# Optimization experiments

Hardware: AMD Instinct MI355X
Metric: run time of the kernel (lower is better)

The kernel has to match this reference:

```python
import jax, jax.numpy as jnp
import numpy as np

L, D, FF, H, S, B = 6, 512, 2048, 8, 1024, 4
DH = D // H
EPS = 1e-5


def setup_inputs() -> dict:
    key = jax.random.key(0)
    ks = jax.random.split(key, 8)
    sd = 1.0 / np.sqrt(D)
    sf = 1.0 / np.sqrt(FF)
    return {
        'src': jax.random.normal(ks[0], (S, B, D), jnp.float32),
        'pos': jax.random.normal(ks[1], (S, B, D), jnp.float32) * 0.02,
        'Wq': jax.random.normal(ks[2], (L, D, D), jnp.float32) * sd,
        'bq': jnp.zeros((L, D), jnp.float32),
        'Wk': jax.random.normal(ks[3], (L, D, D), jnp.float32) * sd,
        'bk': jnp.zeros((L, D), jnp.float32),
        'Wv': jax.random.normal(ks[4], (L, D, D), jnp.float32) * sd,
        'bv': jnp.zeros((L, D), jnp.float32),
        'W1': jax.random.normal(ks[5], (L, D, FF), jnp.float32) * sd,
        'b1': jnp.zeros((L, FF), jnp.float32),
        'W2': jax.random.normal(ks[6], (L, FF, D), jnp.float32) * sf,
        'b2': jnp.zeros((L, D), jnp.float32),
        'ln1_g': jnp.ones((L, D), jnp.float32),
        'ln1_b': jnp.zeros((L, D), jnp.float32),
        'ln2_g': jnp.ones((L, D), jnp.float32),
        'ln2_b': jnp.zeros((L, D), jnp.float32),
        'lnf_g': jnp.ones((D,), jnp.float32),
        'lnf_b': jnp.zeros((D,), jnp.float32),
    }


def _layernorm(x, g, b):
    m = jnp.mean(x, axis=-1, keepdims=True)
    v = jnp.mean(jnp.square(x - m), axis=-1, keepdims=True)
    return (x - m) * jax.lax.rsqrt(v + EPS) * g + b


def _encoder(src, pos, Wq, bq, Wk, bk, Wv, bv, W1, b1, W2, b2,
             ln1_g, ln1_b, ln2_g, ln2_b, lnf_g, lnf_b):
    # src, pos: (S, B, D). Each layer internally transposes to (B, S, D) and the
    # encoder transposes back; equivalently work in (B, S, D) throughout the loop.
    x = (src + pos).transpose(1, 0, 2)  # (B, S, D)
    scale = 1.0 / np.sqrt(DH)
    for i in range(L):
        # --- self-attention block (pre-norm) ---
        x1 = _layernorm(x, ln1_g[i], ln1_b[i])
        q = (x1 @ Wq[i] + bq[i]).reshape(B, S, H, DH)
        k = (x1 @ Wk[i] + bk[i]).reshape(B, S, H, DH)
        v = (x1 @ Wv[i] + bv[i]).reshape(B, S, H, DH)
        scores = jnp.einsum('bqhd,bkhd->bhqk', q, k) * scale  # (B, H, S, S)
        probs = jax.nn.softmax(scores, axis=-1)
        ctx = jnp.einsum('bhqk,bkhd->bqhd', probs, v).reshape(B, S, D)
        x = x + ctx  # dropout=0.0 -> identity
        # --- feed-forward block (pre-norm) ---
        x2 = _layernorm(x, ln2_g[i], ln2_b[i])
        h = jax.nn.relu(x2 @ W1[i] + b1[i])
        x = x + (h @ W2[i] + b2[i])
    out = x.transpose(1, 0, 2)  # back to (S, B, D)
    return _layernorm(out, lnf_g, lnf_b)


def reference(src, pos, Wq, bq, Wk, bk, Wv, bv, W1, b1, W2, b2,
              ln1_g, ln1_b, ln2_g, ln2_b, lnf_g, lnf_b):
    return _encoder(src, pos, Wq, bq, Wk, bk, Wv, bv, W1, b1, W2, b2,
                    ln1_g, ln1_b, ln2_g, ln2_b, lnf_g, lnf_b)
```

## Files before the change

kernel.cpp:

```cpp
#include <hip/hip_runtime.h>

#define L_LAYERS 6
#define DMODEL 512
#define FFDIM 2048
#define NHEAD 8
#define SEQ 1024
#define BATCH 4
#define DHEAD 64
#define MROWS (BATCH*SEQ)

typedef __attribute__((ext_vector_type(4))) float f32x4;
typedef __attribute__((ext_vector_type(8))) unsigned short u16x8;
typedef __attribute__((ext_vector_type(8))) __bf16 bf16x8;

#define DEV static __device__ __forceinline__

DEV unsigned short f32_to_bf16(float f) {
  unsigned int u = __float_as_uint(f);
  u += 0x7fffu + ((u >> 16) & 1u);
  return (unsigned short)(u >> 16);
}
DEV float bf16_to_f32(unsigned short h) {
  return __uint_as_float(((unsigned int)h) << 16);
}
DEV f32x4 mfma_bf16(u16x8 a, u16x8 b, f32x4 c) {
  return __builtin_amdgcn_mfma_f32_16x16x32_bf16(
      __builtin_bit_cast(bf16x8, a), __builtin_bit_cast(bf16x8, b), c, 0, 0, 0);
}
DEV void gload16(const unsigned short* g, unsigned short* l) {
  __builtin_amdgcn_global_load_lds(
      (const __attribute__((address_space(1))) unsigned int*)g,
      (__attribute__((address_space(3))) unsigned int*)l, 16, 0, 0);
}

__global__ __launch_bounds__(256) void k_transpose(const float* __restrict__ Win,
                                                   unsigned short* __restrict__ Wout,
                                                   int K, int N) {
  __shared__ float t[32][33];
  Win  += (size_t)blockIdx.z * K * N;
  Wout += (size_t)blockIdx.z * K * N;
  int n0 = blockIdx.x * 32, k0 = blockIdx.y * 32;
  int lx = threadIdx.x & 31, ly = threadIdx.x >> 5;
  #pragma unroll
  for (int r = 0; r < 32; r += 8)
    t[ly + r][lx] = Win[(size_t)(k0 + ly + r) * N + n0 + lx];
  __syncthreads();
  #pragma unroll
  for (int r = 0; r < 32; r += 8)
    Wout[(size_t)(n0 + ly + r) * K + k0 + lx] = f32_to_bf16(t[lx][ly + r]);
}

__global__ __launch_bounds__(256) void k_addpos_ln(const float* __restrict__ src,
                                                   const float* __restrict__ pos,
                                                   const float* __restrict__ g,
                                                   const float* __restrict__ be,
                                                   float* __restrict__ x,
                                                   unsigned short* __restrict__ o) {
  int lane = threadIdx.x & 63, wv = threadIdx.x >> 6;
  int row = blockIdx.x * 4 + wv;
  int b = row >> 10, ss = row & (SEQ-1);
  const float* sr = src + (size_t)(ss*BATCH + b) * DMODEL + lane * 8;
  const float* pr = pos + (size_t)(ss*BATCH + b) * DMODEL + lane * 8;
  f32x4 v0 = *(const f32x4*)sr + *(const f32x4*)pr;
  f32x4 v1 = *(const f32x4*)(sr + 4) + *(const f32x4*)(pr + 4);
  float* xr = x + (size_t)row * DMODEL + lane * 8;
  *(f32x4*)xr = v0;
  *(f32x4*)(xr + 4) = v1;
  float s  = v0.x+v0.y+v0.z+v0.w + v1.x+v1.y+v1.z+v1.w;
  float s2 = v0.x*v0.x+v0.y*v0.y+v0.z*v0.z+v0.w*v0.w
           + v1.x*v1.x+v1.y*v1.y+v1.z*v1.z+v1.w*v1.w;
  #pragma unroll
  for (int off = 1; off < 64; off <<= 1) { s += __shfl_xor(s, off); s2 += __shfl_xor(s2, off); }
  float mean = s * (1.0f/DMODEL);
  float var  = s2 * (1.0f/DMODEL) - mean*mean;
  float rs = rsqrtf(var + 1e-5f);
  const float* gp = g + lane*8; const float* bp = be + lane*8;
  f32x4 g0 = *(const f32x4*)gp, g1 = *(const f32x4*)(gp+4);
  f32x4 b0 = *(const f32x4*)bp, b1v = *(const f32x4*)(bp+4);
  u16x8 r;
  r[0] = f32_to_bf16((v0.x-mean)*rs*g0.x + b0.x);
  r[1] = f32_to_bf16((v0.y-mean)*rs*g0.y + b0.y);
  r[2] = f32_to_bf16((v0.z-mean)*rs*g0.z + b0.z);
  r[3] = f32_to_bf16((v0.w-mean)*rs*g0.w + b0.w);
  r[4] = f32_to_bf16((v1.x-mean)*rs*g1.x + b1v.x);
  r[5] = f32_to_bf16((v1.y-mean)*rs*g1.y + b1v.y);
  r[6] = f32_to_bf16((v1.z-mean)*rs*g1.z + b1v.z);
  r[7] = f32_to_bf16((v1.w-mean)*rs*g1.w + b1v.w);
  *(u16x8*)(o + (size_t)row * DMODEL + lane * 8) = r;
}

__global__ __launch_bounds__(256) void k_ln_bf16(const float* __restrict__ x,
                                                 const float* __restrict__ g,
                                                 const float* __restrict__ be,
                                                 unsigned short* __restrict__ o) {
  int lane = threadIdx.x & 63, wv = threadIdx.x >> 6;
  int row = blockIdx.x * 4 + wv;
  const float* xr = x + (size_t)row * DMODEL + lane * 8;
  f32x4 v0 = *(const f32x4*)xr, v1 = *(const f32x4*)(xr + 4);
  float s  = v0.x+v0.y+v0.z+v0.w + v1.x+v1.y+v1.z+v1.w;
  float s2 = v0.x*v0.x+v0.y*v0.y+v0.z*v0.z+v0.w*v0.w
           + v1.x*v1.x+v1.y*v1.y+v1.z*v1.z+v1.w*v1.w;
  #pragma unroll
  for (int off = 1; off < 64; off <<= 1) { s += __shfl_xor(s, off); s2 += __shfl_xor(s2, off); }
  float mean = s * (1.0f/DMODEL);
  float var  = s2 * (1.0f/DMODEL) - mean*mean;
  float rs = rsqrtf(var + 1e-5f);
  const float* gp = g + lane*8; const float* bp = be + lane*8;
  f32x4 g0 = *(const f32x4*)gp, g1 = *(const f32x4*)(gp+4);
  f32x4 b0 = *(const f32x4*)bp, b1v = *(const f32x4*)(bp+4);
  u16x8 r;
  r[0] = f32_to_bf16((v0.x-mean)*rs*g0.x + b0.x);
  r[1] = f32_to_bf16((v0.y-mean)*rs*g0.y + b0.y);
  r[2] = f32_to_bf16((v0.z-mean)*rs*g0.z + b0.z);
  r[3] = f32_to_bf16((v0.w-mean)*rs*g0.w + b0.w);
  r[4] = f32_to_bf16((v1.x-mean)*rs*g1.x + b1v.x);
  r[5] = f32_to_bf16((v1.y-mean)*rs*g1.y + b1v.y);
  r[6] = f32_to_bf16((v1.z-mean)*rs*g1.z + b1v.z);
  r[7] = f32_to_bf16((v1.w-mean)*rs*g1.w + b1v.w);
  *(u16x8*)(o + (size_t)row * DMODEL + lane * 8) = r;
}

__global__ __launch_bounds__(256) void k_ln_final(const float* __restrict__ x,
                                                  const float* __restrict__ g,
                                                  const float* __restrict__ be,
                                                  float* __restrict__ out) {
  int lane = threadIdx.x & 63, wv = threadIdx.x >> 6;
  int row = blockIdx.x * 4 + wv;
  const float* xr = x + (size_t)row * DMODEL + lane * 8;
  f32x4 v0 = *(const f32x4*)xr, v1 = *(const f32x4*)(xr + 4);
  float s  = v0.x+v0.y+v0.z+v0.w + v1.x+v1.y+v1.z+v1.w;
  float s2 = v0.x*v0.x+v0.y*v0.y+v0.z*v0.z+v0.w*v0.w
           + v1.x*v1.x+v1.y*v1.y+v1.z*v1.z+v1.w*v1.w;
  #pragma unroll
  for (int off = 1; off < 64; off <<= 1) { s += __shfl_xor(s, off); s2 += __shfl_xor(s2, off); }
  float mean = s * (1.0f/DMODEL);
  float var  = s2 * (1.0f/DMODEL) - mean*mean;
  float rs = rsqrtf(var + 1e-5f);
  const float* gp = g + lane*8; const float* bp = be + lane*8;
  f32x4 g0 = *(const f32x4*)gp, g1 = *(const f32x4*)(gp+4);
  f32x4 b0 = *(const f32x4*)bp, b1v = *(const f32x4*)(bp+4);
  int b = row >> 10, ss = row & (SEQ-1);
  float* orow = out + (size_t)(ss*BATCH + b) * DMODEL + lane * 8;
  f32x4 o0, o1;
  o0.x = (v0.x-mean)*rs*g0.x + b0.x;  o0.y = (v0.y-mean)*rs*g0.y + b0.y;
  o0.z = (v0.z-mean)*rs*g0.z + b0.z;  o0.w = (v0.w-mean)*rs*g0.w + b0.w;
  o1.x = (v1.x-mean)*rs*g1.x + b1v.x; o1.y = (v1.y-mean)*rs*g1.y + b1v.y;
  o1.z = (v1.z-mean)*rs*g1.z + b1v.z; o1.w = (v1.w-mean)*rs*g1.w + b1v.w;
  *(f32x4*)orow = o0;
  *(f32x4*)(orow + 4) = o1;
}

#define BM 128
#define BN 128
#define BKK 32

DEV void gemm_core(const unsigned short* __restrict__ A,
                   const unsigned short* __restrict__ Bt,
                   int K, int m0, int n0,
                   unsigned short* As, unsigned short* Bs, f32x4 acc[4][4]) {
  const int tid = threadIdx.x;
  const int lane = tid & 63;
  const int w = tid >> 6;
  const int wr = w >> 1, wc = w & 1;
  const int l15 = lane & 15;
  const int ko = (lane >> 4) * 8;
  const int rl = lane >> 2;
  const int cc = (lane & 3) * 8;
  for (int kb = 0; kb < K; kb += BKK) {
    #pragma unroll
    for (int i = 0; i < 2; ++i) {
      int r0 = w * 32 + i * 16;
      gload16(A  + (size_t)(m0 + r0 + rl) * K + kb + cc, As + r0 * BKK);
      gload16(Bt + (size_t)(n0 + r0 + rl) * K + kb + cc, Bs + r0 * BKK);
    }
    __syncthreads();
    u16x8 af[4], bfr[4];
    #pragma unroll
    for (int m = 0; m < 4; ++m) af[m]  = *(const u16x8*)(As + (wr*64 + m*16 + l15) * BKK + ko);
    #pragma unroll
    for (int n = 0; n < 4; ++n) bfr[n] = *(const u16x8*)(Bs + (wc*64 + n*16 + l15) * BKK + ko);
    #pragma unroll
    for (int m = 0; m < 4; ++m)
      #pragma unroll
      for (int n = 0; n < 4; ++n)
        acc[m][n] = mfma_bf16(af[m], bfr[n], acc[m][n]);
    __syncthreads();
  }
}

__global__ __launch_bounds__(256) void k_gemm_qkv(
    const unsigned short* __restrict__ x1,
    const unsigned short* __restrict__ WqT, const unsigned short* __restrict__ WkT,
    const unsigned short* __restrict__ WvT,
    const float* __restrict__ bq, const float* __restrict__ bk, const float* __restrict__ bv,
    unsigned short* __restrict__ qo, unsigned short* __restrict__ ko2,
    unsigned short* __restrict__ vo) {
  __shared__ __align__(16) unsigned short As[BM*BKK];
  __shared__ __align__(16) unsigned short Bs[64*BKK];
  const int tid = threadIdx.x;
  const int lane = tid & 63;
  const int w = tid >> 6;
  const int wr = w >> 1, wc = w & 1;
  const int l15 = lane & 15;
  const int ko = (lane >> 4) * 8;
  const int rl = lane >> 2;
  const int cc = (lane & 3) * 8;
  const int m0 = blockIdx.x * BM;
  const int mat = blockIdx.y >> 3;
  const int n0 = (blockIdx.y & 7) * 64;
  const unsigned short* Bt = (mat == 0) ? WqT : ((mat == 1) ? WkT : WvT);
  const float* bias        = (mat == 0) ? bq  : ((mat == 1) ? bk  : bv);
  unsigned short* out      = (mat == 0) ? qo  : ((mat == 1) ? ko2 : vo);
  const float osc = (mat == 0) ? 0.125f : 1.0f;
  f32x4 acc[4][2];
  #pragma unroll
  for (int m = 0; m < 4; ++m)
    #pragma unroll
    for (int n = 0; n < 2; ++n) acc[m][n] = 0.0f;
  for (int kb = 0; kb < DMODEL; kb += BKK) {
    #pragma unroll
    for (int i = 0; i < 2; ++i) {
      int r0 = w * 32 + i * 16;
      gload16(x1 + (size_t)(m0 + r0 + rl) * DMODEL + kb + cc, As + r0 * BKK);
    }
    {
      int r0 = w * 16;
      gload16(Bt + (size_t)(n0 + r0 + rl) * DMODEL + kb + cc, Bs + r0 * BKK);
    }
    __syncthreads();
    u16x8 af[4], bfr[2];
    #pragma unroll
    for (int m = 0; m < 4; ++m) af[m]  = *(const u16x8*)(As + (wr*64 + m*16 + l15) * BKK + ko);
    #pragma unroll
    for (int n = 0; n < 2; ++n) bfr[n] = *(const u16x8*)(Bs + (wc*32 + n*16 + l15) * BKK + ko);
    #pragma unroll
    for (int m = 0; m < 4; ++m)
      #pragma unroll
      for (int n = 0; n < 2; ++n)
        acc[m][n] = mfma_bf16(af[m], bfr[n], acc[m][n]);
    __syncthreads();
  }
  const int g = lane >> 4;
  #pragma unroll
  for (int m = 0; m < 4; ++m) {
    #pragma unroll
    for (int n = 0; n < 2; ++n) {
      int col = n0 + wc*32 + n*16 + l15;
      int hh = col >> 6, dh = col & 63;
      float bval = bias[col];
      #pragma unroll
      for (int i = 0; i < 4; ++i) {
        int row = m0 + wr*64 + m*16 + g*4 + i;
        int bb = row >> 10, ss = row & (SEQ-1);
        size_t oidx;
        if (mat == 2)
          oidx = ((((size_t)(bb*NHEAD + hh)) * DHEAD + dh) << 10) + ss;
        else
          oidx = ((((size_t)(bb*NHEAD + hh)) << 10) + ss) * DHEAD + dh;
        out[oidx] = f32_to_bf16((acc[m][n][i] + bval) * osc);
      }
    }
  }
}

__global__ __launch_bounds__(256) void k_gemm_ffn1(
    const unsigned short* __restrict__ x1, const unsigned short* __restrict__ W1T,
    const float* __restrict__ b1, unsigned short* __restrict__ h) {
  __shared__ __align__(16) unsigned short As[BM*BKK];
  __shared__ __align__(16) unsigned short Bs[BN*BKK];
  int m0 = blockIdx.x * BM, n0 = blockIdx.y * BN;
  f32x4 acc[4][4];
  #pragma unroll
  for (int m = 0; m < 4; ++m)
    #pragma unroll
    for (int n = 0; n < 4; ++n) acc[m][n] = 0.0f;
  gemm_core(x1, W1T, DMODEL, m0, n0, As, Bs, acc);
  const int lane = threadIdx.x & 63;
  const int w = threadIdx.x >> 6; const int wr = w >> 1, wc = w & 1;
  #pragma unroll
  for (int m = 0; m < 4; ++m) {
    #pragma unroll
    for (int n = 0; n < 4; ++n) {
      int col = n0 + wc*64 + n*16 + (lane & 15);
      float bval = b1[col];
      #pragma unroll
      for (int i = 0; i < 4; ++i) {
        int row = m0 + wr*64 + m*16 + (lane >> 4)*4 + i;
        h[(size_t)row * FFDIM + col] = f32_to_bf16(fmaxf(acc[m][n][i] + bval, 0.0f));
      }
    }
  }
}

__global__ __launch_bounds__(256) void k_gemm_ffn2(
    const unsigned short* __restrict__ h, const unsigned short* __restrict__ W2T,
    const float* __restrict__ b2, float* __restrict__ x) {
  __shared__ __align__(16) unsigned short As[64*BKK];
  __shared__ __align__(16) unsigned short Bs[64*BKK];
  const int tid = threadIdx.x;
  const int lane = tid & 63;
  const int w = tid >> 6;
  const int wr = w >> 1, wc = w & 1;
  const int l15 = lane & 15;
  const int ko = (lane >> 4) * 8;
  const int rl = lane >> 2;
  const int cc = (lane & 3) * 8;
  const int m0 = blockIdx.x * 64, n0 = blockIdx.y * 64;
  f32x4 acc[2][2];
  #pragma unroll
  for (int m = 0; m < 2; ++m)
    #pragma unroll
    for (int n = 0; n < 2; ++n) acc[m][n] = 0.0f;
  for (int kb = 0; kb < FFDIM; kb += BKK) {
    int r0 = w * 16;
    gload16(h   + (size_t)(m0 + r0 + rl) * FFDIM + kb + cc, As + r0 * BKK);
    gload16(W2T + (size_t)(n0 + r0 + rl) * FFDIM + kb + cc, Bs + r0 * BKK);
    __syncthreads();
    u16x8 af[2], bfr[2];
    #pragma unroll
    for (int m = 0; m < 2; ++m) af[m]  = *(const u16x8*)(As + (wr*32 + m*16 + l15) * BKK + ko);
    #pragma unroll
    for (int n = 0; n < 2; ++n) bfr[n] = *(const u16x8*)(Bs + (wc*32 + n*16 + l15) * BKK + ko);
    #pragma unroll
    for (int m = 0; m < 2; ++m)
      #pragma unroll
      for (int n = 0; n < 2; ++n)
        acc[m][n] = mfma_bf16(af[m], bfr[n], acc[m][n]);
    __syncthreads();
  }
  const int g = lane >> 4;
  #pragma unroll
  for (int m = 0; m < 2; ++m) {
    #pragma unroll
    for (int n = 0; n < 2; ++n) {
      int col = n0 + wc*32 + n*16 + l15;
      float bval = b2[col];
      #pragma unroll
      for (int i = 0; i < 4; ++i) {
        int row = m0 + wr*32 + m*16 + g*4 + i;
        size_t idx = (size_t)row * DMODEL + col;
        x[idx] = x[idx] + acc[m][n][i] + bval;
      }
    }
  }
}

#define KVBLK 64
#define KP 72
#define NT (SEQ/KVBLK)
#define RESCALE_THR 8.0f

__global__ __launch_bounds__(512) void k_attn_mfma(
    const unsigned short* __restrict__ qb,
    const unsigned short* __restrict__ kb,
    const unsigned short* __restrict__ vtb,
    float* __restrict__ x) {
  __shared__ __align__(16) unsigned short Kl[2][KVBLK*KP];
  __shared__ __align__(16) unsigned short Vl[2][DHEAD*KP];
  __shared__ __align__(16) unsigned short Pl[8*16*KP];
  const int tid = threadIdx.x;
  const int w = tid >> 6, lane = tid & 63;
  const int c = lane & 15, g = lane >> 4;
  const int bh = blockIdx.x, qt = blockIdx.y;
  const int qw = qt * 128 + w * 16;
  const int sr = tid >> 3;
  const int scb = (tid & 7) * 8;

  const unsigned short* kbase = kb + (size_t)bh * SEQ * DHEAD;
  const unsigned short* vbase = vtb + (size_t)bh * DHEAD * SEQ;

  u16x8 qf[2];
  {
    const unsigned short* qrow = qb + ((size_t)bh * SEQ + qw + c) * DHEAD;
    qf[0] = *(const u16x8*)(qrow + g * 8);
    qf[1] = *(const u16x8*)(qrow + 32 + g * 8);
  }
  f32x4 aco[4];
  #pragma unroll
  for (int n = 0; n < 4; ++n) aco[n] = 0.0f;
  float m_r = -1e30f, l_r = 0.0f;

  u16x8 kr0, vr0;
  kr0 = *(const u16x8*)(kbase + (size_t)sr * DHEAD + scb);
  vr0 = *(const u16x8*)(vbase + (size_t)sr * SEQ + scb);
  *(u16x8*)(Kl[0] + sr * KP + scb) = kr0;
  *(u16x8*)(Vl[0] + sr * KP + scb) = vr0;
  __syncthreads();

  int cur = 0;
  for (int t = 0; t < NT; ++t) {
    if (t < NT - 1) {
      int kn = (t + 1) * KVBLK;
      kr0 = *(const u16x8*)(kbase + (size_t)(kn + sr) * DHEAD + scb);
      vr0 = *(const u16x8*)(vbase + (size_t)sr * SEQ + kn + scb);
    }
    const unsigned short* Kt = Kl[cur];
    const unsigned short* Vt = Vl[cur];

    f32x4 s[4];
    #pragma unroll
    for (int n = 0; n < 4; ++n) s[n] = 0.0f;
    #pragma unroll
    for (int n = 0; n < 4; ++n) {
      #pragma unroll
      for (int kk = 0; kk < 2; ++kk) {
        u16x8 kf = *(const u16x8*)(Kt + (n * 16 + c) * KP + kk * 32 + g * 8);
        s[n] = mfma_bf16(kf, qf[kk], s[n]);
      }
    }

    float mx01 = fmaxf(fmaxf(s[0][0], s[0][1]), fmaxf(s[0][2], s[0][3]));
    float mx1  = fmaxf(fmaxf(s[1][0], s[1][1]), fmaxf(s[1][2], s[1][3]));
    float mx2  = fmaxf(fmaxf(s[2][0], s[2][1]), fmaxf(s[2][2], s[2][3]));
    float mx3  = fmaxf(fmaxf(s[3][0], s[3][1]), fmaxf(s[3][2], s[3][3]));
    float mx = fmaxf(fmaxf(mx01, mx1), fmaxf(mx2, mx3));
    mx = fmaxf(mx, __shfl_xor(mx, 16));
    mx = fmaxf(mx, __shfl_xor(mx, 32));

    bool grow = !__all(mx <= m_r + RESCALE_THR);
    float corr = 1.0f;
    if (grow) {
      float mn = fmaxf(m_r, mx);
      corr = __expf(m_r - mn);
      m_r = mn;
    }

    float p[4][4];
    float ps = 0.0f;
    #pragma unroll
    for (int n = 0; n < 4; ++n) {
      #pragma unroll
      for (int i = 0; i < 4; ++i) {
        float pv = __expf(s[n][i] - m_r);
        p[n][i] = pv;
        ps += pv;
      }
    }
    ps += __shfl_xor(ps, 16);
    ps += __shfl_xor(ps, 32);
    l_r = l_r * corr + ps;

    {
      unsigned short* prow = Pl + (w * 16 + c) * KP;
      #pragma unroll
      for (int n = 0; n < 4; ++n) {
        unsigned int pk0 = (unsigned int)f32_to_bf16(p[n][0])
                         | ((unsigned int)f32_to_bf16(p[n][1]) << 16);
        unsigned int pk1 = (unsigned int)f32_to_bf16(p[n][2])
                         | ((unsigned int)f32_to_bf16(p[n][3]) << 16);
        *(unsigned int*)(prow + n * 16 + g * 4)     = pk0;
        *(unsigned int*)(prow + n * 16 + g * 4 + 2) = pk1;
      }
    }

    if (grow) {
      #pragma unroll
      for (int i = 0; i < 4; ++i) {
        float cq = __shfl(corr, g * 4 + i);
        #pragma unroll
        for (int n = 0; n < 4; ++n) aco[n][i] *= cq;
      }
    }

    u16x8 pa[2];
    pa[0] = *(const u16x8*)(Pl + (w * 16 + c) * KP + g * 8);
    pa[1] = *(const u16x8*)(Pl + (w * 16 + c) * KP + 32 + g * 8);
    #pragma unroll
    for (int n = 0; n < 4; ++n) {
      #pragma unroll
      for (int kk = 0; kk < 2; ++kk) {
        u16x8 vf = *(const u16x8*)(Vt + (n * 16 + c) * KP + kk * 32 + g * 8);
        aco[n] = mfma_bf16(pa[kk], vf, aco[n]);
      }
    }

    if (t < NT - 1) {
      unsigned short* Kn = Kl[cur ^ 1];
      unsigned short* Vn = Vl[cur ^ 1];
      *(u16x8*)(Kn + sr * KP + scb) = kr0;
      *(u16x8*)(Vn + sr * KP + scb) = vr0;
      __syncthreads();
    }
    cur ^= 1;
  }

  const int b = bh >> 3, h = bh & 7;
  #pragma unroll
  for (int i = 0; i < 4; ++i) {
    float lq = __shfl(l_r, g * 4 + i);
    float inv = 1.0f / lq;
    int q = qw + g * 4 + i;
    float* xr = x + ((size_t)b * SEQ + q) * DMODEL + h * DHEAD;
    #pragma unroll
    for (int n = 0; n < 4; ++n)
      xr[n * 16 + c] += aco[n][i] * inv;
  }
}

extern "C" void kernel_launch(void* const* d_in, const int* in_sizes, int n_in,
                              void* d_out, int out_size, void* d_ws, size_t ws_size,
                              hipStream_t stream) {
  const float* src  = (const float*)d_in[0];
  const float* pos  = (const float*)d_in[1];
  const float* Wq   = (const float*)d_in[2];
  const float* bq   = (const float*)d_in[3];
  const float* Wk   = (const float*)d_in[4];
  const float* bk   = (const float*)d_in[5];
  const float* Wv   = (const float*)d_in[6];
  const float* bv   = (const float*)d_in[7];
  const float* W1   = (const float*)d_in[8];
  const float* b1   = (const float*)d_in[9];
  const float* W2   = (const float*)d_in[10];
  const float* b2   = (const float*)d_in[11];
  const float* ln1g = (const float*)d_in[12];
  const float* ln1b = (const float*)d_in[13];
  const float* ln2g = (const float*)d_in[14];
  const float* ln2b = (const float*)d_in[15];
  const float* lnfg = (const float*)d_in[16];
  const float* lnfb = (const float*)d_in[17];

  char* p = (char*)d_ws;
  float* x = (float*)p;                      p += (size_t)MROWS * DMODEL * 4;
  unsigned short* x1 = (unsigned short*)p;   p += (size_t)MROWS * DMODEL * 2;
  unsigned short* qb = (unsigned short*)p;   p += (size_t)MROWS * DMODEL * 2;
  unsigned short* kbuf = (unsigned short*)p; p += (size_t)MROWS * DMODEL * 2;
  unsigned short* vtbuf = (unsigned short*)p; p += (size_t)MROWS * DMODEL * 2;
  unsigned short* hbuf = (unsigned short*)p; p += (size_t)MROWS * FFDIM * 2;
  unsigned short* WqT = (unsigned short*)p;  p += (size_t)L_LAYERS * DMODEL * DMODEL * 2;
  unsigned short* WkT = (unsigned short*)p;  p += (size_t)L_LAYERS * DMODEL * DMODEL * 2;
  unsigned short* WvT = (unsigned short*)p;  p += (size_t)L_LAYERS * DMODEL * DMODEL * 2;
  unsigned short* W1T = (unsigned short*)p;  p += (size_t)L_LAYERS * DMODEL * FFDIM * 2;
  unsigned short* W2T = (unsigned short*)p;  p += (size_t)L_LAYERS * DMODEL * FFDIM * 2;

  k_transpose<<<dim3(16,16,6), 256, 0, stream>>>(Wq, WqT, DMODEL, DMODEL);
  k_transpose<<<dim3(16,16,6), 256, 0, stream>>>(Wk, WkT, DMODEL, DMODEL);
  k_transpose<<<dim3(16,16,6), 256, 0, stream>>>(Wv, WvT, DMODEL, DMODEL);
  k_transpose<<<dim3(64,16,6), 256, 0, stream>>>(W1, W1T, DMODEL, FFDIM);
  k_transpose<<<dim3(16,64,6), 256, 0, stream>>>(W2, W2T, FFDIM, DMODEL);

  for (int l = 0; l < L_LAYERS; ++l) {
    if (l == 0)
      k_addpos_ln<<<1024, 256, 0, stream>>>(src, pos, ln1g, ln1b, x, x1);
    else
      k_ln_bf16<<<1024, 256, 0, stream>>>(x, ln1g + l*DMODEL, ln1b + l*DMODEL, x1);
    k_gemm_qkv<<<dim3(32,24), 256, 0, stream>>>(
        x1,
        WqT + (size_t)l*DMODEL*DMODEL, WkT + (size_t)l*DMODEL*DMODEL, WvT + (size_t)l*DMODEL*DMODEL,
        bq + l*DMODEL, bk + l*DMODEL, bv + l*DMODEL,
        qb, kbuf, vtbuf);
    k_attn_mfma<<<dim3(32,8), 512, 0, stream>>>(qb, kbuf, vtbuf, x);
    k_ln_bf16<<<1024, 256, 0, stream>>>(x, ln2g + l*DMODEL, ln2b + l*DMODEL, x1);
    k_gemm_ffn1<<<dim3(32,16), 256, 0, stream>>>(x1, W1T + (size_t)l*DMODEL*FFDIM, b1 + l*FFDIM, hbuf);
    k_gemm_ffn2<<<dim3(64,8), 256, 0, stream>>>(hbuf, W2T + (size_t)l*DMODEL*FFDIM, b2 + l*DMODEL, x);
  }
  k_ln_final<<<1024, 256, 0, stream>>>(x, lnfg, lnfb, (float*)d_out);
}
```

Before: 559.9 us.

## Switch attention kernel to 32x32x16 MFMA with 32-query waves

Rewrites the flash-attention kernel to use 32x32x16 bf16 MFMA instructions, with each of 4 waves handling 32 query rows instead of 8 waves handling 16. Row max and sum reductions need fewer cross-lane shuffles, and K/V fragments in LDS are reused across more queries per wave. The block shrinks to 256 threads and each thread stages two 16-byte chunks per tile. In exchange each wave holds more accumulator registers, and there are fewer waves per block to hide latency.

```diff
diff --git a/kernel.cpp b/kernel.cpp
--- a/kernel.cpp
+++ b/kernel.cpp
@@ -10,6 +10,7 @@
 #define MROWS (BATCH*SEQ)
 
 typedef __attribute__((ext_vector_type(4))) float f32x4;
+typedef __attribute__((ext_vector_type(16))) float f32x16;
 typedef __attribute__((ext_vector_type(8))) unsigned short u16x8;
 typedef __attribute__((ext_vector_type(8))) __bf16 bf16x8;
 
@@ -25,6 +26,10 @@
 }
 DEV f32x4 mfma_bf16(u16x8 a, u16x8 b, f32x4 c) {
   return __builtin_amdgcn_mfma_f32_16x16x32_bf16(
+      __builtin_bit_cast(bf16x8, a), __builtin_bit_cast(bf16x8, b), c, 0, 0, 0);
+}
+DEV f32x16 mfma32(u16x8 a, u16x8 b, f32x16 c) {
+  return __builtin_amdgcn_mfma_f32_32x32x16_bf16(
       __builtin_bit_cast(bf16x8, a), __builtin_bit_cast(bf16x8, b), c, 0, 0, 0);
 }
 DEV void gload16(const unsigned short* g, unsigned short* l) {
@@ -350,71 +355,75 @@
 #define NT (SEQ/KVBLK)
 #define RESCALE_THR 8.0f
 
-__global__ __launch_bounds__(512) void k_attn_mfma(
+__global__ __launch_bounds__(256) void k_attn_mfma(
     const unsigned short* __restrict__ qb,
     const unsigned short* __restrict__ kb,
     const unsigned short* __restrict__ vtb,
     float* __restrict__ x) {
   __shared__ __align__(16) unsigned short Kl[2][KVBLK*KP];
   __shared__ __align__(16) unsigned short Vl[2][DHEAD*KP];
-  __shared__ __align__(16) unsigned short Pl[8*16*KP];
+  __shared__ __align__(16) unsigned short Pl[4*32*KP];
   const int tid = threadIdx.x;
   const int w = tid >> 6, lane = tid & 63;
-  const int c = lane & 15, g = lane >> 4;
+  const int l31 = lane & 31, h5 = lane >> 5;
   const int bh = blockIdx.x, qt = blockIdx.y;
-  const int qw = qt * 128 + w * 16;
-  const int sr = tid >> 3;
-  const int scb = (tid & 7) * 8;
+  const int qw = qt * 128 + w * 32;
+  const int sr = tid >> 2;
+  const int sc = (tid & 3) * 16;
 
   const unsigned short* kbase = kb + (size_t)bh * SEQ * DHEAD;
   const unsigned short* vbase = vtb + (size_t)bh * DHEAD * SEQ;
 
-  u16x8 qf[2];
+  u16x8 qf[4];
   {
-    const unsigned short* qrow = qb + ((size_t)bh * SEQ + qw + c) * DHEAD;
-    qf[0] = *(const u16x8*)(qrow + g * 8);
-    qf[1] = *(const u16x8*)(qrow + 32 + g * 8);
-  }
-  f32x4 aco[4];
-  #pragma unroll
-  for (int n = 0; n < 4; ++n) aco[n] = 0.0f;
+    const unsigned short* qrow = qb + ((size_t)bh * SEQ + qw + l31) * DHEAD;
+    #pragma unroll
+    for (int ks = 0; ks < 4; ++ks)
+      qf[ks] = *(const u16x8*)(qrow + ks * 16 + h5 * 8);
+  }
+  f32x16 aco0 = 0.0f, aco1 = 0.0f;
   float m_r = -1e30f, l_r = 0.0f;
 
-  u16x8 kr0, vr0;
-  kr0 = *(const u16x8*)(kbase + (size_t)sr * DHEAD + scb);
-  vr0 = *(const u16x8*)(vbase + (size_t)sr * SEQ + scb);
-  *(u16x8*)(Kl[0] + sr * KP + scb) = kr0;
-  *(u16x8*)(Vl[0] + sr * KP + scb) = vr0;
+  u16x8 kra0, kra1, vra0, vra1;
+  kra0 = *(const u16x8*)(kbase + (size_t)sr * DHEAD + sc);
+  kra1 = *(const u16x8*)(kbase + (size_t)sr * DHEAD + sc + 8);
+  vra0 = *(const u16x8*)(vbase + (size_t)sr * SEQ + sc);
+  vra1 = *(const u16x8*)(vbase + (size_t)sr * SEQ + sc + 8);
+  *(u16x8*)(Kl[0] + sr * KP + sc)     = kra0;
+  *(u16x8*)(Kl[0] + sr * KP + sc + 8) = kra1;
+  *(u16x8*)(Vl[0] + sr * KP + sc)     = vra0;
+  *(u16x8*)(Vl[0] + sr * KP + sc + 8) = vra1;
   __syncthreads();
 
   int cur = 0;
   for (int t = 0; t < NT; ++t) {
     if (t < NT - 1) {
       int kn = (t + 1) * KVBLK;
-      kr0 = *(const u16x8*)(kbase + (size_t)(kn + sr) * DHEAD + scb);
-      vr0 = *(const u16x8*)(vbase + (size_t)sr * SEQ + kn + scb);
+      kra0 = *(const u16x8*)(kbase + (size_t)(kn + sr) * DHEAD + sc);
+      kra1 = *(const u16x8*)(kbase + (size_t)(kn + sr) * DHEAD + sc + 8);
+      vra0 = *(const u16x8*)(vbase + (size_t)sr * SEQ + kn + sc);
+      vra1 = *(const u16x8*)(vbase + (size_t)sr * SEQ + kn + sc + 8);
     }
     const unsigned short* Kt = Kl[cur];
     const unsigned short* Vt = Vl[cur];
 
-    f32x4 s[4];
-    #pragma unroll
-    for (int n = 0; n < 4; ++n) s[n] = 0.0f;
-    #pragma unroll
-    for (int n = 0; n < 4; ++n) {
-      #pragma unroll
-      for (int kk = 0; kk < 2; ++kk) {
-        u16x8 kf = *(const u16x8*)(Kt + (n * 16 + c) * KP + kk * 32 + g * 8);
-        s[n] = mfma_bf16(kf, qf[kk], s[n]);
-      }
-    }
-
-    float mx01 = fmaxf(fmaxf(s[0][0], s[0][1]), fmaxf(s[0][2], s[0][3]));
-    float mx1  = fmaxf(fmaxf(s[1][0], s[1][1]), fmaxf(s[1][2], s[1][3]));
-    float mx2  = fmaxf(fmaxf(s[2][0], s[2][1]), fmaxf(s[2][2], s[2][3]));
-    float mx3  = fmaxf(fmaxf(s[3][0], s[3][1]), fmaxf(s[3][2], s[3][3]));
-    float mx = fmaxf(fmaxf(mx01, mx1), fmaxf(mx2, mx3));
-    mx = fmaxf(mx, __shfl_xor(mx, 16));
+    f32x16 s0 = 0.0f, s1 = 0.0f;
+    #pragma unroll
+    for (int ks = 0; ks < 4; ++ks) {
+      u16x8 kf = *(const u16x8*)(Kt + l31 * KP + ks * 16 + h5 * 8);
+      s0 = mfma32(kf, qf[ks], s0);
+    }
+    #pragma unroll
+    for (int ks = 0; ks < 4; ++ks) {
+      u16x8 kf = *(const u16x8*)(Kt + (32 + l31) * KP + ks * 16 + h5 * 8);
+      s1 = mfma32(kf, qf[ks], s1);
+    }
+
+    float mx = s0[0];
+    #pragma unroll
+    for (int r = 1; r < 16; ++r) mx = fmaxf(mx, s0[r]);
+    #pragma unroll
+    for (int r = 0; r < 16; ++r) mx = fmaxf(mx, s1[r]);
     mx = fmaxf(mx, __shfl_xor(mx, 32));
 
     bool grow = !__all(mx <= m_r + RESCALE_THR);
@@ -425,60 +434,57 @@
       m_r = mn;
     }
 
-    float p[4][4];
     float ps = 0.0f;
-    #pragma unroll
-    for (int n = 0; n < 4; ++n) {
-      #pragma unroll
-      for (int i = 0; i < 4; ++i) {
-        float pv = __expf(s[n][i] - m_r);
-        p[n][i] = pv;
-        ps += pv;
+    {
+      unsigned short* prow = Pl + (w * 32 + l31) * KP;
+      #pragma unroll
+      for (int rg = 0; rg < 4; ++rg) {
+        int c0 = 8 * rg + 4 * h5;
+        float a0 = __expf(s0[4*rg]   - m_r), a1 = __expf(s0[4*rg+1] - m_r);
+        float a2 = __expf(s0[4*rg+2] - m_r), a3 = __expf(s0[4*rg+3] - m_r);
+        ps += (a0 + a1) + (a2 + a3);
+        *(unsigned int*)(prow + c0)     = (unsigned)f32_to_bf16(a0) | ((unsigned)f32_to_bf16(a1) << 16);
+        *(unsigned int*)(prow + c0 + 2) = (unsigned)f32_to_bf16(a2) | ((unsigned)f32_to_bf16(a3) << 16);
+        float b0 = __expf(s1[4*rg]   - m_r), b1 = __expf(s1[4*rg+1] - m_r);
+        float b2 = __expf(s1[4*rg+2] - m_r), b3 = __expf(s1[4*rg+3] - m_r);
+        ps += (b0 + b1) + (b2 + b3);
+        *(unsigned int*)(prow + 32 + c0)     = (unsigned)f32_to_bf16(b0) | ((unsigned)f32_to_bf16(b1) << 16);
+        *(unsigned int*)(prow + 32 + c0 + 2) = (unsigned)f32_to_bf16(b2) | ((unsigned)f32_to_bf16(b3) << 16);
       }
     }
-    ps += __shfl_xor(ps, 16);
     ps += __shfl_xor(ps, 32);
     l_r = l_r * corr + ps;
 
-    {
-      unsigned short* prow = Pl + (w * 16 + c) * KP;
-      #pragma unroll
-      for (int n = 0; n < 4; ++n) {
-        unsigned int pk0 = (unsigned int)f32_to_bf16(p[n][0])
-                         | ((unsigned int)f32_to_bf16(p[n][1]) << 16);
-        unsigned int pk1 = (unsigned int)f32_to_bf16(p[n][2])
-                         | ((unsigned int)f32_to_bf16(p[n][3]) << 16);
-        *(unsigned int*)(prow + n * 16 + g * 4)     = pk0;
-        *(unsigned int*)(prow + n * 16 + g * 4 + 2) = pk1;
+    if (grow) {
+      #pragma unroll
+      for (int r = 0; r < 16; ++r) {
+        float cq = __shfl(corr, (r & 3) + 8 * (r >> 2) + 4 * h5);
+        aco0[r] *= cq; aco1[r] *= cq;
       }
     }
 
-    if (grow) {
-      #pragma unroll
-      for (int i = 0; i < 4; ++i) {
-        float cq = __shfl(corr, g * 4 + i);
-        #pragma unroll
-        for (int n = 0; n < 4; ++n) aco[n][i] *= cq;
-      }
-    }
-
-    u16x8 pa[2];
-    pa[0] = *(const u16x8*)(Pl + (w * 16 + c) * KP + g * 8);
-    pa[1] = *(const u16x8*)(Pl + (w * 16 + c) * KP + 32 + g * 8);
-    #pragma unroll
-    for (int n = 0; n < 4; ++n) {
-      #pragma unroll
-      for (int kk = 0; kk < 2; ++kk) {
-        u16x8 vf = *(const u16x8*)(Vt + (n * 16 + c) * KP + kk * 32 + g * 8);
-        aco[n] = mfma_bf16(pa[kk], vf, aco[n]);
-      }
+    u16x8 pa[4];
+    #pragma unroll
+    for (int kvs = 0; kvs < 4; ++kvs)
+      pa[kvs] = *(const u16x8*)(Pl + (w * 32 + l31) * KP + kvs * 16 + h5 * 8);
+    #pragma unroll
+    for (int kvs = 0; kvs < 4; ++kvs) {
+      u16x8 vf = *(const u16x8*)(Vt + l31 * KP + kvs * 16 + h5 * 8);
+      aco0 = mfma32(pa[kvs], vf, aco0);
+    }
+    #pragma unroll
+    for (int kvs = 0; kvs < 4; ++kvs) {
+      u16x8 vf = *(const u16x8*)(Vt + (32 + l31) * KP + kvs * 16 + h5 * 8);
+      aco1 = mfma32(pa[kvs], vf, aco1);
     }
 
     if (t < NT - 1) {
       unsigned short* Kn = Kl[cur ^ 1];
       unsigned short* Vn = Vl[cur ^ 1];
-      *(u16x8*)(Kn + sr * KP + scb) = kr0;
-      *(u16x8*)(Vn + sr * KP + scb) = vr0;
+      *(u16x8*)(Kn + sr * KP + sc)     = kra0;
+      *(u16x8*)(Kn + sr * KP + sc + 8) = kra1;
+      *(u16x8*)(Vn + sr * KP + sc)     = vra0;
+      *(u16x8*)(Vn + sr * KP + sc + 8) = vra1;
       __syncthreads();
     }
     cur ^= 1;
@@ -486,14 +492,13 @@
 
   const int b = bh >> 3, h = bh & 7;
   #pragma unroll
-  for (int i = 0; i < 4; ++i) {
-    float lq = __shfl(l_r, g * 4 + i);
-    float inv = 1.0f / lq;
-    int q = qw + g * 4 + i;
+  for (int r = 0; r < 16; ++r) {
+    int crow = (r & 3) + 8 * (r >> 2) + 4 * h5;
+    float inv = 1.0f / __shfl(l_r, crow);
+    int q = qw + crow;
     float* xr = x + ((size_t)b * SEQ + q) * DMODEL + h * DHEAD;
-    #pragma unroll
-    for (int n = 0; n < 4; ++n)
-      xr[n * 16 + c] += aco[n][i] * inv;
+    xr[l31]      += aco0[r] * inv;
+    xr[32 + l31] += aco1[r] * inv;
   }
 }
 
@@ -548,7 +553,7 @@
         WqT + (size_t)l*DMODEL*DMODEL, WkT + (size_t)l*DMODEL*DMODEL, WvT + (size_t)l*DMODEL*DMODEL,
         bq + l*DMODEL, bk + l*DMODEL, bv + l*DMODEL,
         qb, kbuf, vtbuf);
-    k_attn_mfma<<<dim3(32,8), 512, 0, stream>>>(qb, kbuf, vtbuf, x);
+    k_attn_mfma<<<dim3(32,8), 256, 0, stream>>>(qb, kbuf, vtbuf, x);
     k_ln_bf16<<<1024, 256, 0, stream>>>(x, ln2g + l*DMODEL, ln2b + l*DMODEL, x1);
     k_gemm_ffn1<<<dim3(32,16), 256, 0, stream>>>(x1, W1T + (size_t)l*DMODEL*FFDIM, b1 + l*FFDIM, hbuf);
     k_gemm_ffn2<<<dim3(64,8), 256, 0, stream>>>(hbuf, W2T + (size_t)l*DMODEL*FFDIM, b2 + l*DMODEL, x);
```

After: 564.7 us. No clear change (+0.9%).
